# Performance work log

Hardware: AMD Instinct MI355X
Metric: run time of the kernel (lower is better)

## Reference

```python
import jax, jax.numpy as jnp
import numpy as np

EMB = 768
HEADS = 8
HEAD_DIM = EMB // HEADS
SCALE = HEAD_DIM ** -0.5


def setup_inputs() -> dict:
    key = jax.random.key(0)
    ks = jax.random.split(key, 9)
    s = 0.02
    return {
        "x": jax.random.normal(ks[0], (2, 4096, EMB), dtype=jnp.float32),
        "Wq": jax.random.normal(ks[1], (EMB, EMB), dtype=jnp.float32) * s,
        "bq": jax.random.normal(ks[2], (EMB,), dtype=jnp.float32) * s,
        "Wk": jax.random.normal(ks[3], (EMB, EMB), dtype=jnp.float32) * s,
        "bk": jax.random.normal(ks[4], (EMB,), dtype=jnp.float32) * s,
        "Wv": jax.random.normal(ks[5], (EMB, EMB), dtype=jnp.float32) * s,
        "bv": jax.random.normal(ks[6], (EMB,), dtype=jnp.float32) * s,
        "Wo": jax.random.normal(ks[7], (EMB, EMB), dtype=jnp.float32) * s,
        "bo": jax.random.normal(ks[8], (EMB,), dtype=jnp.float32) * s,
    }


def reference(x, Wq, bq, Wk, bk, Wv, bv, Wo, bo):
    b, n, _ = x.shape
    # torch Linear: y = x @ W.T + b
    def split_heads(y):  # [b, n, emb] -> [b, h, n, d]
        return y.reshape(b, n, HEADS, HEAD_DIM).transpose(0, 2, 1, 3)

    q = split_heads(x @ Wq.T + bq)
    k = split_heads(x @ Wk.T + bk)
    v = split_heads(x @ Wv.T + bv)
    # scores [b, h, q, k]; source applies scaling inside softmax input
    scores = jnp.einsum('bhqd,bhkd->bhqk', q, k) * SCALE
    weight = jax.nn.softmax(scores, axis=-1)
    out = jnp.einsum('bhqk,bhkd->bhqd', weight, v)
    out = out.transpose(0, 2, 1, 3).reshape(b, n, EMB)
    return out @ Wo.T + bo
```

## Files before the change

### kernel.cpp

```cpp
#include <hip/hip_runtime.h>


typedef __bf16 bf16;
typedef __attribute__((ext_vector_type(2))) float f32x2;
typedef __attribute__((ext_vector_type(4))) float f32x4;
typedef __attribute__((ext_vector_type(16))) float f32x16;
typedef __attribute__((ext_vector_type(8))) __bf16 bf16x8;
typedef __attribute__((ext_vector_type(4))) __bf16 bf16x4;
typedef __attribute__((ext_vector_type(4))) unsigned u32x4;

#define EMB 768
#define SEQ 4096
#define NB 2
#define NHEADS 8
#define HD 96
#define BHTOT (NB * NHEADS)
#define MTOT (NB * SEQ)
#define QSCALE 0.14724241052735512f

#define AS1 __attribute__((address_space(1)))
#define AS3 __attribute__((address_space(3)))

__global__ __launch_bounds__(256) void cast_f32_bf16(const float* __restrict__ in,
                                                     bf16* __restrict__ out) {
  const int i = (blockIdx.x * 256 + threadIdx.x) * 4;
  const f32x4 v = *reinterpret_cast<const f32x4*>(in + i);
  bf16x4 o;
  o[0] = (bf16)v[0]; o[1] = (bf16)v[1]; o[2] = (bf16)v[2]; o[3] = (bf16)v[3];
  *reinterpret_cast<bf16x4*>(out + i) = o;
}

__global__ __launch_bounds__(256) void cast_w4(const float* __restrict__ w0,
                                               const float* __restrict__ w1,
                                               const float* __restrict__ w2,
                                               const float* __restrict__ w3,
                                               bf16* __restrict__ o0,
                                               bf16* __restrict__ o1,
                                               bf16* __restrict__ o2,
                                               bf16* __restrict__ o3) {
  const float* w = (blockIdx.y == 0) ? w0 : (blockIdx.y == 1) ? w1 : (blockIdx.y == 2) ? w2 : w3;
  bf16* o = (blockIdx.y == 0) ? o0 : (blockIdx.y == 1) ? o1 : (blockIdx.y == 2) ? o2 : o3;
  const int i = (blockIdx.x * 256 + threadIdx.x) * 4;
  const f32x4 v = *reinterpret_cast<const f32x4*>(w + i);
  bf16x4 ob;
  ob[0] = (bf16)v[0]; ob[1] = (bf16)v[1]; ob[2] = (bf16)v[2]; ob[3] = (bf16)v[3];
  *reinterpret_cast<bf16x4*>(o + i) = ob;
}

template <int MODE>
__global__ __launch_bounds__(256) void gemm_bt(const bf16* __restrict__ A,
                                               const bf16* __restrict__ B,
                                               const float* __restrict__ b0,
                                               const float* __restrict__ b1,
                                               const float* __restrict__ b2,
                                               void* __restrict__ out,
                                               void* __restrict__ outK) {
  constexpr int K = EMB;
  __shared__ bf16 As[128 * 32];
  __shared__ bf16 Bs[128 * 32];
  const int tid = threadIdx.x;
  const int lane = tid & 63;
  const int wid = tid >> 6;
  const int wr = wid >> 1, wc = wid & 1;
  const int l15 = lane & 15, l4 = lane >> 4;
  const int rowBase = blockIdx.y * 128;
  const int colBase = blockIdx.x * 128;

  f32x4 acc[4][4] = {};

  for (int kt = 0; kt < K / 32; ++kt) {
    const int kb = kt * 32;
#pragma unroll
    for (int i = 0; i < 2; ++i) {
      const int c = (wid * 2 + i) * 64 + lane;
      const int row = c >> 2, cc = c & 3;
      const bf16* ga = A + (size_t)(rowBase + row) * K + kb + cc * 8;
      const bf16* gb = B + (size_t)(colBase + row) * K + kb + cc * 8;
      __builtin_amdgcn_global_load_lds(
          (const AS1 void*)ga,
          (AS3 void*)(As + (size_t)(wid * 2 + i) * 512), 16, 0, 0);
      __builtin_amdgcn_global_load_lds(
          (const AS1 void*)gb,
          (AS3 void*)(Bs + (size_t)(wid * 2 + i) * 512), 16, 0, 0);
    }
    __syncthreads();
    bf16x8 af[4], bfr[4];
#pragma unroll
    for (int t = 0; t < 4; ++t) {
      af[t]  = *reinterpret_cast<const bf16x8*>(As + (wr * 64 + t * 16 + l15) * 32 + l4 * 8);
      bfr[t] = *reinterpret_cast<const bf16x8*>(Bs + (wc * 64 + t * 16 + l15) * 32 + l4 * 8);
    }
#pragma unroll
    for (int mt = 0; mt < 4; ++mt)
#pragma unroll
      for (int nt = 0; nt < 4; ++nt)
        acc[mt][nt] = __builtin_amdgcn_mfma_f32_16x16x32_bf16(af[mt], bfr[nt], acc[mt][nt], 0, 0, 0);
    __syncthreads();
  }

#pragma unroll
  for (int mt = 0; mt < 4; ++mt) {
#pragma unroll
    for (int nt = 0; nt < 4; ++nt) {
      const int gn = colBase + wc * 64 + nt * 16 + l15;
      if (MODE == 0) {
        const int mm = gn / 768;
        const int g7 = gn - mm * 768;
        const int h = g7 / HD, d = g7 - h * HD;
        const float* bp = (mm == 0) ? b0 : (mm == 1) ? b1 : b2;
        const float bv = bp[g7];
        const float sc = (mm == 0) ? QSCALE : 1.f;
#pragma unroll
        for (int r = 0; r < 4; ++r) {
          const int gm = rowBase + wr * 64 + mt * 16 + l4 * 4 + r;
          const int b = gm >> 12, n = gm & (SEQ - 1);
          const float v = (acc[mt][nt][r] + bv) * sc;
          if (mm == 1) {
            ((bf16*)outK)[((size_t)(b * NHEADS + h) * SEQ + n) * 128 +
                          (((d >> 3) ^ (n & 7)) << 3) + (d & 7)] = (bf16)v;
          } else {
            bf16* dst = (bf16*)out + (mm == 2 ? (size_t)MTOT * EMB : 0);
            dst[((size_t)(b * NHEADS + h) * SEQ + n) * HD + d] = (bf16)v;
          }
        }
      } else {
        const float bv = b0[gn];
#pragma unroll
        for (int r = 0; r < 4; ++r) {
          const int gm = rowBase + wr * 64 + mt * 16 + l4 * 4 + r;
          ((float*)out)[(size_t)gm * EMB + gn] = acc[mt][nt][r] + bv;
        }
      }
    }
  }
}

__global__ __launch_bounds__(256) void transpose_v(const bf16* __restrict__ v,
                                                   bf16* __restrict__ vt) {
  __shared__ bf16 T[96][72];
  const int bh = blockIdx.y;
  const int n0 = blockIdx.x * 64;
  const int tid = threadIdx.x;
#pragma unroll
  for (int i = 0; i < 3; ++i) {
    const int c = i * 256 + tid;
    const int n = c / 12, cc = c % 12;
    const bf16x8 val = *reinterpret_cast<const bf16x8*>(
        v + ((size_t)bh * SEQ + n0 + n) * HD + cc * 8);
#pragma unroll
    for (int j = 0; j < 8; ++j) T[cc * 8 + j][n] = val[j];
  }
  __syncthreads();
#pragma unroll
  for (int i = 0; i < 3; ++i) {
    const int c = i * 256 + tid;
    const int d = c >> 3, nc = c & 7;
    const int s0i = (nc >> 1) * 16 + (nc & 1) * 4;
    const bf16x4 lo = *reinterpret_cast<const bf16x4*>(&T[d][s0i]);
    const bf16x4 hi = *reinterpret_cast<const bf16x4*>(&T[d][s0i + 8]);
    const bf16x8 val = __builtin_shufflevector(lo, hi, 0, 1, 2, 3, 4, 5, 6, 7);
    const int pc = nc ^ (d & 7);
    *reinterpret_cast<bf16x8*>(vt + ((size_t)bh * HD + d) * SEQ + n0 + pc * 8) = val;
  }
}

template <int SPLIT>
__global__ __launch_bounds__(256, 2) void attn_fwd(const bf16* __restrict__ q,
                                                   const bf16* __restrict__ ksw,
                                                   const bf16* __restrict__ vt,
                                                   void* __restrict__ outp,
                                                   float* __restrict__ lsum) {
  __shared__ bf16 Ks[2][64 * 128];
  __shared__ bf16 Vts[2][96 * 64];
  const int tid = threadIdx.x;
  const int lane = tid & 63;
  const int wid = tid >> 6;
  const int l31 = lane & 31, lhi = lane >> 5;
  const int lin = (blockIdx.z * gridDim.y + blockIdx.y) * gridDim.x + blockIdx.x;
  const int nblk = 256 * SPLIT;
  const int cpx = nblk >> 3;
  const int l2 = (lin & 7) * cpx + (lin >> 3);
  const int qblk = l2 & 15;
  const int z = (SPLIT == 2) ? ((l2 >> 4) & 1) : 0;
  const int bh = (SPLIT == 2) ? (l2 >> 5) : (l2 >> 4);
  const int q0 = qblk * 256 + wid * 64;
  constexpr int NT = SEQ / 64 / SPLIT;
  const int kv00 = z * NT * 64;
  const size_t headq = (size_t)bh * SEQ * HD;
  const bf16* kg = ksw + (size_t)bh * SEQ * 128;
  const bf16* vg = vt + (size_t)bh * (size_t)HD * SEQ;

  const bf16* kp = kg + (size_t)kv00 * 128 + (size_t)tid * 8;
  const bf16* vp = vg + (size_t)(tid >> 3) * SEQ + kv00 + (tid & 7) * 8;

  int krd[12], vrd[12];
#pragma unroll
  for (int kib = 0; kib < 2; ++kib)
#pragma unroll
    for (int dc = 0; dc < 6; ++dc) {
      const int row = kib * 32 + l31;
      krd[kib * 6 + dc] = (row * 128 + (((dc * 2 + lhi) ^ (l31 & 7)) * 8)) * 2;
    }
#pragma unroll
  for (int db = 0; db < 3; ++db)
#pragma unroll
    for (int kb = 0; kb < 4; ++kb) {
      const int row = db * 32 + l31;
      vrd[db * 4 + kb] = (row * 64 + (((kb * 2 + lhi) ^ (l31 & 7)) * 8)) * 2;
    }

  bf16x8 qf[2][6];
#pragma unroll
  for (int g = 0; g < 2; ++g)
#pragma unroll
    for (int dc = 0; dc < 6; ++dc)
      qf[g][dc] = *reinterpret_cast<const bf16x8*>(
          q + headq + (size_t)(q0 + g * 32 + l31) * HD + dc * 16 + lhi * 8);

  f32x16 oacc[2][3] = {};
  float lrun[2] = {0.f, 0.f};

#pragma unroll
  for (int i = 0; i < 4; ++i)
    __builtin_amdgcn_global_load_lds((const AS1 void*)(kp + i * 2048),
                                     (AS3 void*)(&Ks[0][i * 2048 + tid * 8]), 16, 0, 0);
#pragma unroll
  for (int i = 0; i < 3; ++i)
    __builtin_amdgcn_global_load_lds((const AS1 void*)(vp + (size_t)i * 32 * SEQ),
                                     (AS3 void*)(&Vts[0][i * 2048 + tid * 8]), 16, 0, 0);
  kp += 8192;
  vp += 64;
  __syncthreads();

  for (int kt = 0; kt < NT; ++kt) {
    const int cur = kt & 1;
    if (kt < NT - 1) {
#pragma unroll
      for (int i = 0; i < 4; ++i)
        __builtin_amdgcn_global_load_lds((const AS1 void*)(kp + i * 2048),
                                         (AS3 void*)(&Ks[cur ^ 1][i * 2048 + tid * 8]), 16, 0, 0);
#pragma unroll
      for (int i = 0; i < 3; ++i)
        __builtin_amdgcn_global_load_lds((const AS1 void*)(vp + (size_t)i * 32 * SEQ),
                                         (AS3 void*)(&Vts[cur ^ 1][i * 2048 + tid * 8]), 16, 0, 0);
      kp += 8192;
      vp += 64;
    }
    const char* ksb = (const char*)Ks[cur];
    const char* vsb = (const char*)Vts[cur];

    bf16x8 pf[2][4];
#pragma unroll
    for (int kib = 0; kib < 2; ++kib) {
      f32x16 s[2] = {};
      __builtin_amdgcn_s_setprio(1);
#pragma unroll
      for (int dc = 0; dc < 6; ++dc) {
        const bf16x8 kf = *reinterpret_cast<const bf16x8*>(ksb + krd[kib * 6 + dc]);
        s[0] = __builtin_amdgcn_mfma_f32_32x32x16_bf16(kf, qf[0][dc], s[0], 0, 0, 0);
        s[1] = __builtin_amdgcn_mfma_f32_32x32x16_bf16(kf, qf[1][dc], s[1], 0, 0, 0);
      }
      __builtin_amdgcn_s_setprio(0);
#pragma unroll
      for (int g = 0; g < 2; ++g) {
        float a0 = 0.f, a1 = 0.f, a2 = 0.f, a3 = 0.f;
#pragma unroll
        for (int i = 0; i < 4; ++i) {
          s[g][4 * i + 0] = __builtin_amdgcn_exp2f(s[g][4 * i + 0]); a0 += s[g][4 * i + 0];
          s[g][4 * i + 1] = __builtin_amdgcn_exp2f(s[g][4 * i + 1]); a1 += s[g][4 * i + 1];
          s[g][4 * i + 2] = __builtin_amdgcn_exp2f(s[g][4 * i + 2]); a2 += s[g][4 * i + 2];
          s[g][4 * i + 3] = __builtin_amdgcn_exp2f(s[g][4 * i + 3]); a3 += s[g][4 * i + 3];
        }
        lrun[g] += (a0 + a1) + (a2 + a3);
        unsigned c[8];
#pragma unroll
        for (int i = 0; i < 8; ++i)
          asm("v_cvt_pk_bf16_f32 %0, %1, %2"
              : "=v"(c[i]) : "v"(s[g][2 * i]), "v"(s[g][2 * i + 1]));
        const u32x4 wa = {c[0], c[1], c[2], c[3]};
        const u32x4 wb = {c[4], c[5], c[6], c[7]};
        pf[g][kib * 2 + 0] = __builtin_bit_cast(bf16x8, wa);
        pf[g][kib * 2 + 1] = __builtin_bit_cast(bf16x8, wb);
      }
    }

    __builtin_amdgcn_s_setprio(1);
#pragma unroll
    for (int kb = 0; kb < 4; ++kb) {
#pragma unroll
      for (int db = 0; db < 3; ++db) {
        const bf16x8 vf = *reinterpret_cast<const bf16x8*>(vsb + vrd[db * 4 + kb]);
        oacc[0][db] = __builtin_amdgcn_mfma_f32_32x32x16_bf16(vf, pf[0][kb], oacc[0][db], 0, 0, 0);
        oacc[1][db] = __builtin_amdgcn_mfma_f32_32x32x16_bf16(vf, pf[1][kb], oacc[1][db], 0, 0, 0);
      }
    }
    __builtin_amdgcn_s_setprio(0);

    __syncthreads();
  }

  const int b = bh >> 3, h = bh & 7;
#pragma unroll
  for (int g = 0; g < 2; ++g) {
    float lr = lrun[g];
    lr += __shfl_xor(lr, 32, 64);
    const int n = q0 + g * 32 + l31;
    if (SPLIT == 2) {
      float* po = (float*)outp + (size_t)z * ((size_t)BHTOT * SEQ * HD) +
                  ((size_t)bh * SEQ + n) * HD;
#pragma unroll
      for (int db = 0; db < 3; ++db)
#pragma unroll
        for (int i = 0; i < 8; ++i) {
          const int r = 2 * i;
          const int d = db * 32 + (r & 3) + 8 * (r >> 2) + 4 * lhi;
          f32x2 w = {oacc[g][db][r], oacc[g][db][r + 1]};
          *reinterpret_cast<f32x2*>(po + d) = w;
        }
      if (lhi == 0) lsum[(size_t)z * BHTOT * SEQ + (size_t)bh * SEQ + n] = lr;
    } else {
      const float inv = 1.f / lr;
      bf16* obase = (bf16*)outp + (size_t)(b * SEQ + n) * EMB + h * HD;
#pragma unroll
      for (int db = 0; db < 3; ++db)
#pragma unroll
        for (int i = 0; i < 8; ++i) {
          const int r = 2 * i;
          const int d = db * 32 + (r & 3) + 8 * (r >> 2) + 4 * lhi;
          unsigned w;
          const float v0 = oacc[g][db][r] * inv, v1 = oacc[g][db][r + 1] * inv;
          asm("v_cvt_pk_bf16_f32 %0, %1, %2" : "=v"(w) : "v"(v0), "v"(v1));
          *reinterpret_cast<unsigned*>(obase + d) = w;
        }
    }
  }
}

__global__ __launch_bounds__(256) void merge_o(const float* __restrict__ p,
                                               const float* __restrict__ ls,
                                               bf16* __restrict__ ao) {
  const int idx = blockIdx.x * 256 + threadIdx.x;
  const size_t PS = (size_t)BHTOT * SEQ * HD;
  const f32x4 a = *reinterpret_cast<const f32x4*>(p + (size_t)idx * 4);
  const f32x4 b2 = *reinterpret_cast<const f32x4*>(p + PS + (size_t)idx * 4);
  const int rest = idx / 24;
  const int d4 = idx - rest * 24;
  const float inv = 1.f / (ls[rest] + ls[BHTOT * SEQ + rest]);
  const int bh = rest >> 12, n = rest & (SEQ - 1);
  const int b = bh >> 3, h = bh & 7;
  bf16x4 o4;
#pragma unroll
  for (int j = 0; j < 4; ++j) o4[j] = (bf16)((a[j] + b2[j]) * inv);
  *reinterpret_cast<bf16x4*>(ao + (size_t)(b * SEQ + n) * EMB + h * HD + d4 * 4) = o4;
}

extern "C" void kernel_launch(void* const* d_in, const int* in_sizes, int n_in,
                              void* d_out, int out_size, void* d_ws, size_t ws_size,
                              hipStream_t stream) {
  const float* x  = (const float*)d_in[0];
  const float* Wq = (const float*)d_in[1];
  const float* bq = (const float*)d_in[2];
  const float* Wk = (const float*)d_in[3];
  const float* bk = (const float*)d_in[4];
  const float* Wv = (const float*)d_in[5];
  const float* bv = (const float*)d_in[6];
  const float* Wo = (const float*)d_in[7];
  const float* bo = (const float*)d_in[8];

  const size_t XN = (size_t)MTOT * EMB;
  const size_t WN = (size_t)EMB * EMB;
  const size_t KSWN = (size_t)BHTOT * SEQ * 128;

  bf16* p = (bf16*)d_ws;
  bf16* xbf  = p; p += XN;
  bf16* wqb  = p; p += WN;
  bf16* wkb  = p; p += WN;
  bf16* wvb  = p; p += WN;
  bf16* wob  = p; p += WN;
  bf16* qb   = p; p += XN;
  bf16* vb   = p; p += XN;
  bf16* kbsw = p; p += KSWN;
  bf16* vtb  = p; p += XN;
  bf16* ao   = p; p += XN;
  const size_t base_bytes = (size_t)((char*)p - (char*)d_ws);
  float* part = (float*)p;
  float* lsum = part + 2 * ((size_t)BHTOT * SEQ * HD);
  const size_t need2 = base_bytes + (2 * (size_t)BHTOT * SEQ * HD) * 4 +
                       (2 * (size_t)BHTOT * SEQ) * 4;
  const bool split2 = (ws_size >= need2);

  cast_f32_bf16<<<XN / 1024, 256, 0, stream>>>(x, xbf);
  cast_w4<<<dim3(WN / 1024, 4), 256, 0, stream>>>(Wq, Wk, Wv, Wo, wqb, wkb, wvb, wob);

  gemm_bt<0><<<dim3(3 * EMB / 128, MTOT / 128), 256, 0, stream>>>(
      xbf, wqb, bq, bk, bv, qb, kbsw);

  transpose_v<<<dim3(SEQ / 64, BHTOT), 256, 0, stream>>>(vb, vtb);

  if (split2) {
    attn_fwd<2><<<dim3(16, 16, 2), 256, 0, stream>>>(qb, kbsw, vtb, part, lsum);
    merge_o<<<(BHTOT * SEQ * HD / 4) / 256, 256, 0, stream>>>(part, lsum, ao);
  } else {
    attn_fwd<1><<<dim3(16, 16, 1), 256, 0, stream>>>(qb, kbsw, vtb, ao, nullptr);
  }

  gemm_bt<1><<<dim3(EMB / 128, MTOT / 128), 256, 0, stream>>>(
      ao, wob, bo, nullptr, nullptr, d_out, nullptr);
}
```

Baseline: 211.0 us.

## Halve attention KV tile to 32 and add 4-way KV split

Shrinks each attention iteration's K/V tile from 64 to 32 keys, with a matching V-transpose swizzle and LDS read offsets. This halves LDS use and registers per block. Adds a SPLIT=4 path, used when workspace allows, that splits the KV sequence across four blocks per query tile, and generalizes merge_o to sum four partials. The aim is more parallelism and occupancy, at the cost of twice as many barriers per key, more partial-output traffic and a heavier merge.

```diff
diff --git a/kernel.cpp b/kernel.cpp
--- a/kernel.cpp
+++ b/kernel.cpp
@@ -159,7 +159,7 @@
     const bf16x4 lo = *reinterpret_cast<const bf16x4*>(&T[d][s0i]);
     const bf16x4 hi = *reinterpret_cast<const bf16x4*>(&T[d][s0i + 8]);
     const bf16x8 val = __builtin_shufflevector(lo, hi, 0, 1, 2, 3, 4, 5, 6, 7);
-    const int pc = nc ^ (d & 7);
+    const int pc = (nc & 4) | ((nc & 3) ^ (d & 3));
     *reinterpret_cast<bf16x8*>(vt + ((size_t)bh * HD + d) * SEQ + n0 + pc * 8) = val;
   }
 }
@@ -170,43 +170,39 @@
                                                    const bf16* __restrict__ vt,
                                                    void* __restrict__ outp,
                                                    float* __restrict__ lsum) {
-  __shared__ bf16 Ks[2][64 * 128];
-  __shared__ bf16 Vts[2][96 * 64];
+  __shared__ bf16 Ks[2][32 * 128];
+  __shared__ bf16 Vts[2][96 * 32];
   const int tid = threadIdx.x;
   const int lane = tid & 63;
   const int wid = tid >> 6;
   const int l31 = lane & 31, lhi = lane >> 5;
   const int lin = (blockIdx.z * gridDim.y + blockIdx.y) * gridDim.x + blockIdx.x;
-  const int nblk = 256 * SPLIT;
-  const int cpx = nblk >> 3;
-  const int l2 = (lin & 7) * cpx + (lin >> 3);
+  constexpr int NBLK = 256 * SPLIT;
+  constexpr int CPX = NBLK >> 3;
+  const int l2 = (lin & 7) * CPX + (lin >> 3);
   const int qblk = l2 & 15;
-  const int z = (SPLIT == 2) ? ((l2 >> 4) & 1) : 0;
-  const int bh = (SPLIT == 2) ? (l2 >> 5) : (l2 >> 4);
+  const int z = (SPLIT == 4) ? ((l2 >> 4) & 3) : (SPLIT == 2) ? ((l2 >> 4) & 1) : 0;
+  const int bh = (SPLIT == 4) ? (l2 >> 6) : (SPLIT == 2) ? (l2 >> 5) : (l2 >> 4);
   const int q0 = qblk * 256 + wid * 64;
-  constexpr int NT = SEQ / 64 / SPLIT;
-  const int kv00 = z * NT * 64;
+  constexpr int NT = SEQ / 32 / SPLIT;
+  const int kv00 = z * NT * 32;
   const size_t headq = (size_t)bh * SEQ * HD;
   const bf16* kg = ksw + (size_t)bh * SEQ * 128;
   const bf16* vg = vt + (size_t)bh * (size_t)HD * SEQ;
 
   const bf16* kp = kg + (size_t)kv00 * 128 + (size_t)tid * 8;
-  const bf16* vp = vg + (size_t)(tid >> 3) * SEQ + kv00 + (tid & 7) * 8;
-
-  int krd[12], vrd[12];
-#pragma unroll
-  for (int kib = 0; kib < 2; ++kib)
-#pragma unroll
-    for (int dc = 0; dc < 6; ++dc) {
-      const int row = kib * 32 + l31;
-      krd[kib * 6 + dc] = (row * 128 + (((dc * 2 + lhi) ^ (l31 & 7)) * 8)) * 2;
-    }
+  const bf16* vp = vg + (size_t)(tid >> 2) * SEQ + kv00 + (tid & 3) * 8;
+
+  int krd[6], vrd[6];
+#pragma unroll
+  for (int dc = 0; dc < 6; ++dc)
+    krd[dc] = (l31 * 128 + (((dc * 2 + lhi) ^ (l31 & 7)) * 8)) * 2;
 #pragma unroll
   for (int db = 0; db < 3; ++db)
 #pragma unroll
-    for (int kb = 0; kb < 4; ++kb) {
+    for (int kb = 0; kb < 2; ++kb) {
       const int row = db * 32 + l31;
-      vrd[db * 4 + kb] = (row * 64 + (((kb * 2 + lhi) ^ (l31 & 7)) * 8)) * 2;
+      vrd[db * 2 + kb] = (row * 32 + (((kb * 2 + lhi) ^ (l31 & 3)) * 8)) * 2;
     }
 
   bf16x8 qf[2][6];
@@ -221,75 +217,75 @@
   float lrun[2] = {0.f, 0.f};
 
 #pragma unroll
-  for (int i = 0; i < 4; ++i)
+  for (int i = 0; i < 2; ++i)
     __builtin_amdgcn_global_load_lds((const AS1 void*)(kp + i * 2048),
                                      (AS3 void*)(&Ks[0][i * 2048 + tid * 8]), 16, 0, 0);
-#pragma unroll
-  for (int i = 0; i < 3; ++i)
-    __builtin_amdgcn_global_load_lds((const AS1 void*)(vp + (size_t)i * 32 * SEQ),
-                                     (AS3 void*)(&Vts[0][i * 2048 + tid * 8]), 16, 0, 0);
-  kp += 8192;
-  vp += 64;
+  __builtin_amdgcn_global_load_lds((const AS1 void*)(vp),
+                                   (AS3 void*)(&Vts[0][tid * 8]), 16, 0, 0);
+  if (tid < 128)
+    __builtin_amdgcn_global_load_lds((const AS1 void*)(vp + (size_t)64 * SEQ),
+                                     (AS3 void*)(&Vts[0][2048 + tid * 8]), 16, 0, 0);
+  kp += 4096;
+  vp += 32;
   __syncthreads();
 
   for (int kt = 0; kt < NT; ++kt) {
     const int cur = kt & 1;
     if (kt < NT - 1) {
 #pragma unroll
-      for (int i = 0; i < 4; ++i)
+      for (int i = 0; i < 2; ++i)
         __builtin_amdgcn_global_load_lds((const AS1 void*)(kp + i * 2048),
                                          (AS3 void*)(&Ks[cur ^ 1][i * 2048 + tid * 8]), 16, 0, 0);
-#pragma unroll
-      for (int i = 0; i < 3; ++i)
-        __builtin_amdgcn_global_load_lds((const AS1 void*)(vp + (size_t)i * 32 * SEQ),
-                                         (AS3 void*)(&Vts[cur ^ 1][i * 2048 + tid * 8]), 16, 0, 0);
-      kp += 8192;
-      vp += 64;
+      __builtin_amdgcn_global_load_lds((const AS1 void*)(vp),
+                                       (AS3 void*)(&Vts[cur ^ 1][tid * 8]), 16, 0, 0);
+      if (tid < 128)
+        __builtin_amdgcn_global_load_lds((const AS1 void*)(vp + (size_t)64 * SEQ),
+                                         (AS3 void*)(&Vts[cur ^ 1][2048 + tid * 8]), 16, 0, 0);
+      kp += 4096;
+      vp += 32;
     }
     const char* ksb = (const char*)Ks[cur];
     const char* vsb = (const char*)Vts[cur];
 
-    bf16x8 pf[2][4];
-#pragma unroll
-    for (int kib = 0; kib < 2; ++kib) {
-      f32x16 s[2] = {};
-      __builtin_amdgcn_s_setprio(1);
-#pragma unroll
-      for (int dc = 0; dc < 6; ++dc) {
-        const bf16x8 kf = *reinterpret_cast<const bf16x8*>(ksb + krd[kib * 6 + dc]);
-        s[0] = __builtin_amdgcn_mfma_f32_32x32x16_bf16(kf, qf[0][dc], s[0], 0, 0, 0);
-        s[1] = __builtin_amdgcn_mfma_f32_32x32x16_bf16(kf, qf[1][dc], s[1], 0, 0, 0);
+    f32x16 s[2] = {};
+    __builtin_amdgcn_s_setprio(1);
+#pragma unroll
+    for (int dc = 0; dc < 6; ++dc) {
+      const bf16x8 kf = *reinterpret_cast<const bf16x8*>(ksb + krd[dc]);
+      s[0] = __builtin_amdgcn_mfma_f32_32x32x16_bf16(kf, qf[0][dc], s[0], 0, 0, 0);
+      s[1] = __builtin_amdgcn_mfma_f32_32x32x16_bf16(kf, qf[1][dc], s[1], 0, 0, 0);
+    }
+    __builtin_amdgcn_s_setprio(0);
+
+    bf16x8 pf[2][2];
+#pragma unroll
+    for (int g = 0; g < 2; ++g) {
+      float a0 = 0.f, a1 = 0.f, a2 = 0.f, a3 = 0.f;
+#pragma unroll
+      for (int i = 0; i < 4; ++i) {
+        s[g][4 * i + 0] = __builtin_amdgcn_exp2f(s[g][4 * i + 0]); a0 += s[g][4 * i + 0];
+        s[g][4 * i + 1] = __builtin_amdgcn_exp2f(s[g][4 * i + 1]); a1 += s[g][4 * i + 1];
+        s[g][4 * i + 2] = __builtin_amdgcn_exp2f(s[g][4 * i + 2]); a2 += s[g][4 * i + 2];
+        s[g][4 * i + 3] = __builtin_amdgcn_exp2f(s[g][4 * i + 3]); a3 += s[g][4 * i + 3];
       }
-      __builtin_amdgcn_s_setprio(0);
-#pragma unroll
-      for (int g = 0; g < 2; ++g) {
-        float a0 = 0.f, a1 = 0.f, a2 = 0.f, a3 = 0.f;
-#pragma unroll
-        for (int i = 0; i < 4; ++i) {
-          s[g][4 * i + 0] = __builtin_amdgcn_exp2f(s[g][4 * i + 0]); a0 += s[g][4 * i + 0];
-          s[g][4 * i + 1] = __builtin_amdgcn_exp2f(s[g][4 * i + 1]); a1 += s[g][4 * i + 1];
-          s[g][4 * i + 2] = __builtin_amdgcn_exp2f(s[g][4 * i + 2]); a2 += s[g][4 * i + 2];
-          s[g][4 * i + 3] = __builtin_amdgcn_exp2f(s[g][4 * i + 3]); a3 += s[g][4 * i + 3];
-        }
-        lrun[g] += (a0 + a1) + (a2 + a3);
-        unsigned c[8];
-#pragma unroll
-        for (int i = 0; i < 8; ++i)
-          asm("v_cvt_pk_bf16_f32 %0, %1, %2"
-              : "=v"(c[i]) : "v"(s[g][2 * i]), "v"(s[g][2 * i + 1]));
-        const u32x4 wa = {c[0], c[1], c[2], c[3]};
-        const u32x4 wb = {c[4], c[5], c[6], c[7]};
-        pf[g][kib * 2 + 0] = __builtin_bit_cast(bf16x8, wa);
-        pf[g][kib * 2 + 1] = __builtin_bit_cast(bf16x8, wb);
-      }
+      lrun[g] += (a0 + a1) + (a2 + a3);
+      unsigned c[8];
+#pragma unroll
+      for (int i = 0; i < 8; ++i)
+        asm("v_cvt_pk_bf16_f32 %0, %1, %2"
+            : "=v"(c[i]) : "v"(s[g][2 * i]), "v"(s[g][2 * i + 1]));
+      const u32x4 wa = {c[0], c[1], c[2], c[3]};
+      const u32x4 wb = {c[4], c[5], c[6], c[7]};
+      pf[g][0] = __builtin_bit_cast(bf16x8, wa);
+      pf[g][1] = __builtin_bit_cast(bf16x8, wb);
     }
 
     __builtin_amdgcn_s_setprio(1);
 #pragma unroll
-    for (int kb = 0; kb < 4; ++kb) {
+    for (int kb = 0; kb < 2; ++kb) {
 #pragma unroll
       for (int db = 0; db < 3; ++db) {
-        const bf16x8 vf = *reinterpret_cast<const bf16x8*>(vsb + vrd[db * 4 + kb]);
+        const bf16x8 vf = *reinterpret_cast<const bf16x8*>(vsb + vrd[db * 2 + kb]);
         oacc[0][db] = __builtin_amdgcn_mfma_f32_32x32x16_bf16(vf, pf[0][kb], oacc[0][db], 0, 0, 0);
         oacc[1][db] = __builtin_amdgcn_mfma_f32_32x32x16_bf16(vf, pf[1][kb], oacc[1][db], 0, 0, 0);
       }
@@ -305,7 +301,7 @@
     float lr = lrun[g];
     lr += __shfl_xor(lr, 32, 64);
     const int n = q0 + g * 32 + l31;
-    if (SPLIT == 2) {
+    if (SPLIT > 1) {
       float* po = (float*)outp + (size_t)z * ((size_t)BHTOT * SEQ * HD) +
                   ((size_t)bh * SEQ + n) * HD;
 #pragma unroll
@@ -336,21 +332,29 @@
   }
 }
 
+template <int SPLIT>
 __global__ __launch_bounds__(256) void merge_o(const float* __restrict__ p,
                                                const float* __restrict__ ls,
                                                bf16* __restrict__ ao) {
   const int idx = blockIdx.x * 256 + threadIdx.x;
   const size_t PS = (size_t)BHTOT * SEQ * HD;
-  const f32x4 a = *reinterpret_cast<const f32x4*>(p + (size_t)idx * 4);
-  const f32x4 b2 = *reinterpret_cast<const f32x4*>(p + PS + (size_t)idx * 4);
   const int rest = idx / 24;
   const int d4 = idx - rest * 24;
-  const float inv = 1.f / (ls[rest] + ls[BHTOT * SEQ + rest]);
+  f32x4 a = *reinterpret_cast<const f32x4*>(p + (size_t)idx * 4);
+  float l = ls[rest];
+#pragma unroll
+  for (int zz = 1; zz < SPLIT; ++zz) {
+    const f32x4 b2 = *reinterpret_cast<const f32x4*>(p + zz * PS + (size_t)idx * 4);
+#pragma unroll
+    for (int j = 0; j < 4; ++j) a[j] += b2[j];
+    l += ls[(size_t)zz * BHTOT * SEQ + rest];
+  }
+  const float inv = 1.f / l;
   const int bh = rest >> 12, n = rest & (SEQ - 1);
   const int b = bh >> 3, h = bh & 7;
   bf16x4 o4;
 #pragma unroll
-  for (int j = 0; j < 4; ++j) o4[j] = (bf16)((a[j] + b2[j]) * inv);
+  for (int j = 0; j < 4; ++j) o4[j] = (bf16)(a[j] * inv);
   *reinterpret_cast<bf16x4*>(ao + (size_t)(b * SEQ + n) * EMB + h * HD + d4 * 4) = o4;
 }
 
@@ -384,10 +388,11 @@
   bf16* ao   = p; p += XN;
   const size_t base_bytes = (size_t)((char*)p - (char*)d_ws);
   float* part = (float*)p;
-  float* lsum = part + 2 * ((size_t)BHTOT * SEQ * HD);
-  const size_t need2 = base_bytes + (2 * (size_t)BHTOT * SEQ * HD) * 4 +
-                       (2 * (size_t)BHTOT * SEQ) * 4;
-  const bool split2 = (ws_size >= need2);
+  const size_t PS = (size_t)BHTOT * SEQ * HD;
+  float* lsum4 = part + 4 * PS;
+  float* lsum2 = part + 2 * PS;
+  const size_t need4 = base_bytes + 4 * PS * 4 + 4 * (size_t)BHTOT * SEQ * 4;
+  const size_t need2 = base_bytes + 2 * PS * 4 + 2 * (size_t)BHTOT * SEQ * 4;
 
   cast_f32_bf16<<<XN / 1024, 256, 0, stream>>>(x, xbf);
   cast_w4<<<dim3(WN / 1024, 4), 256, 0, stream>>>(Wq, Wk, Wv, Wo, wqb, wkb, wvb, wob);
@@ -397,9 +402,12 @@
 
   transpose_v<<<dim3(SEQ / 64, BHTOT), 256, 0, stream>>>(vb, vtb);
 
-  if (split2) {
-    attn_fwd<2><<<dim3(16, 16, 2), 256, 0, stream>>>(qb, kbsw, vtb, part, lsum);
-    merge_o<<<(BHTOT * SEQ * HD / 4) / 256, 256, 0, stream>>>(part, lsum, ao);
+  if (ws_size >= need4) {
+    attn_fwd<4><<<dim3(16, 16, 4), 256, 0, stream>>>(qb, kbsw, vtb, part, lsum4);
+    merge_o<4><<<(BHTOT * SEQ * HD / 4) / 256, 256, 0, stream>>>(part, lsum4, ao);
+  } else if (ws_size >= need2) {
+    attn_fwd<2><<<dim3(16, 16, 2), 256, 0, stream>>>(qb, kbsw, vtb, part, lsum2);
+    merge_o<2><<<(BHTOT * SEQ * HD / 4) / 256, 256, 0, stream>>>(part, lsum2, ao);
   } else {
     attn_fwd<1><<<dim3(16, 16, 1), 256, 0, stream>>>(qb, kbsw, vtb, ao, nullptr);
   }
```

Result: slower. 233.8 us (+10.8%).

## Software-pipeline QK and PV across KV tiles, triple-buffer V, store bf16 partials

Applied to the files above, without the earlier changes.

Restructures the attention inner loop so each half-tile's QK^T MFMAs are interleaved with the softmax and PV of the previous half-tile, with V moved to a triple buffer so its loads can be issued two tiles ahead. Precomputed LDS offset arrays are dropped and offsets are computed inline. Split-KV partial outputs are now stored as bf16 instead of fp32, halving partial-write and merge traffic, and the merge kernel is vectorised to 8 elements per thread. This costs extra LDS and register pressure and reduces partial-sum precision.

```diff
diff --git a/kernel.cpp b/kernel.cpp
--- a/kernel.cpp
+++ b/kernel.cpp
@@ -2,7 +2,6 @@
 
 
 typedef __bf16 bf16;
-typedef __attribute__((ext_vector_type(2))) float f32x2;
 typedef __attribute__((ext_vector_type(4))) float f32x4;
 typedef __attribute__((ext_vector_type(16))) float f32x16;
 typedef __attribute__((ext_vector_type(8))) __bf16 bf16x8;
@@ -171,15 +170,15 @@
                                                    void* __restrict__ outp,
                                                    float* __restrict__ lsum) {
   __shared__ bf16 Ks[2][64 * 128];
-  __shared__ bf16 Vts[2][96 * 64];
+  __shared__ bf16 Vts[3][96 * 64];
   const int tid = threadIdx.x;
   const int lane = tid & 63;
   const int wid = tid >> 6;
   const int l31 = lane & 31, lhi = lane >> 5;
   const int lin = (blockIdx.z * gridDim.y + blockIdx.y) * gridDim.x + blockIdx.x;
-  const int nblk = 256 * SPLIT;
-  const int cpx = nblk >> 3;
-  const int l2 = (lin & 7) * cpx + (lin >> 3);
+  constexpr int NBLK = 256 * SPLIT;
+  constexpr int CPX = NBLK >> 3;
+  const int l2 = (lin & 7) * CPX + (lin >> 3);
   const int qblk = l2 & 15;
   const int z = (SPLIT == 2) ? ((l2 >> 4) & 1) : 0;
   const int bh = (SPLIT == 2) ? (l2 >> 5) : (l2 >> 4);
@@ -193,22 +192,6 @@
   const bf16* kp = kg + (size_t)kv00 * 128 + (size_t)tid * 8;
   const bf16* vp = vg + (size_t)(tid >> 3) * SEQ + kv00 + (tid & 7) * 8;
 
-  int krd[12], vrd[12];
-#pragma unroll
-  for (int kib = 0; kib < 2; ++kib)
-#pragma unroll
-    for (int dc = 0; dc < 6; ++dc) {
-      const int row = kib * 32 + l31;
-      krd[kib * 6 + dc] = (row * 128 + (((dc * 2 + lhi) ^ (l31 & 7)) * 8)) * 2;
-    }
-#pragma unroll
-  for (int db = 0; db < 3; ++db)
-#pragma unroll
-    for (int kb = 0; kb < 4; ++kb) {
-      const int row = db * 32 + l31;
-      vrd[db * 4 + kb] = (row * 64 + (((kb * 2 + lhi) ^ (l31 & 7)) * 8)) * 2;
-    }
-
   bf16x8 qf[2][6];
 #pragma unroll
   for (int g = 0; g < 2; ++g)
@@ -220,83 +203,109 @@
   f32x16 oacc[2][3] = {};
   float lrun[2] = {0.f, 0.f};
 
-#pragma unroll
-  for (int i = 0; i < 4; ++i)
-    __builtin_amdgcn_global_load_lds((const AS1 void*)(kp + i * 2048),
-                                     (AS3 void*)(&Ks[0][i * 2048 + tid * 8]), 16, 0, 0);
-#pragma unroll
-  for (int i = 0; i < 3; ++i)
-    __builtin_amdgcn_global_load_lds((const AS1 void*)(vp + (size_t)i * 32 * SEQ),
-                                     (AS3 void*)(&Vts[0][i * 2048 + tid * 8]), 16, 0, 0);
-  kp += 8192;
-  vp += 64;
+  auto STAGE_K = [&](int buf) {
+#pragma unroll
+    for (int i = 0; i < 4; ++i)
+      __builtin_amdgcn_global_load_lds((const AS1 void*)(kp + i * 2048),
+                                       (AS3 void*)(&Ks[buf][i * 2048 + tid * 8]), 16, 0, 0);
+    kp += 8192;
+  };
+  auto STAGE_V = [&](int buf) {
+#pragma unroll
+    for (int i = 0; i < 3; ++i)
+      __builtin_amdgcn_global_load_lds((const AS1 void*)(vp + (size_t)i * 32 * SEQ),
+                                       (AS3 void*)(&Vts[buf][i * 2048 + tid * 8]), 16, 0, 0);
+    vp += 64;
+  };
+  auto QKSTEP = [&](const bf16* ksb_, int kib, f32x16& s0, f32x16& s1) {
+    const char* ksb = (const char*)ksb_;
+    __builtin_amdgcn_s_setprio(1);
+#pragma unroll
+    for (int dc = 0; dc < 6; ++dc) {
+      const int off = ((kib * 32 + l31) * 128 + (((dc * 2 + lhi) ^ (l31 & 7)) * 8)) * 2;
+      const bf16x8 kf = *reinterpret_cast<const bf16x8*>(ksb + off);
+      s0 = __builtin_amdgcn_mfma_f32_32x32x16_bf16(kf, qf[0][dc], s0, 0, 0, 0);
+      s1 = __builtin_amdgcn_mfma_f32_32x32x16_bf16(kf, qf[1][dc], s1, 0, 0, 0);
+    }
+    __builtin_amdgcn_s_setprio(0);
+  };
+  auto SMPV = [&](const bf16* vsb_, int kib, f32x16& c0, f32x16& c1) {
+    const char* vsb = (const char*)vsb_;
+    bf16x8 vf[2][3];
+#pragma unroll
+    for (int kb = 0; kb < 2; ++kb)
+#pragma unroll
+      for (int db = 0; db < 3; ++db) {
+        const int off = ((db * 32 + l31) * 64 +
+                         ((((kib * 2 + kb) * 2 + lhi) ^ (l31 & 7)) * 8)) * 2;
+        vf[kb][db] = *reinterpret_cast<const bf16x8*>(vsb + off);
+      }
+    bf16x8 pf0[2], pf1[2];
+    {
+      float a0 = 0.f, a1 = 0.f, a2 = 0.f, a3 = 0.f;
+#pragma unroll
+      for (int i = 0; i < 4; ++i) {
+        c0[4 * i + 0] = __builtin_amdgcn_exp2f(c0[4 * i + 0]); a0 += c0[4 * i + 0];
+        c0[4 * i + 1] = __builtin_amdgcn_exp2f(c0[4 * i + 1]); a1 += c0[4 * i + 1];
+        c0[4 * i + 2] = __builtin_amdgcn_exp2f(c0[4 * i + 2]); a2 += c0[4 * i + 2];
+        c0[4 * i + 3] = __builtin_amdgcn_exp2f(c0[4 * i + 3]); a3 += c0[4 * i + 3];
+      }
+      lrun[0] += (a0 + a1) + (a2 + a3);
+      unsigned c[8];
+#pragma unroll
+      for (int i = 0; i < 8; ++i)
+        asm("v_cvt_pk_bf16_f32 %0, %1, %2" : "=v"(c[i]) : "v"(c0[2 * i]), "v"(c0[2 * i + 1]));
+      const u32x4 wa = {c[0], c[1], c[2], c[3]};
+      const u32x4 wb = {c[4], c[5], c[6], c[7]};
+      pf0[0] = __builtin_bit_cast(bf16x8, wa);
+      pf0[1] = __builtin_bit_cast(bf16x8, wb);
+    }
+    {
+      float a0 = 0.f, a1 = 0.f, a2 = 0.f, a3 = 0.f;
+#pragma unroll
+      for (int i = 0; i < 4; ++i) {
+        c1[4 * i + 0] = __builtin_amdgcn_exp2f(c1[4 * i + 0]); a0 += c1[4 * i + 0];
+        c1[4 * i + 1] = __builtin_amdgcn_exp2f(c1[4 * i + 1]); a1 += c1[4 * i + 1];
+        c1[4 * i + 2] = __builtin_amdgcn_exp2f(c1[4 * i + 2]); a2 += c1[4 * i + 2];
+        c1[4 * i + 3] = __builtin_amdgcn_exp2f(c1[4 * i + 3]); a3 += c1[4 * i + 3];
+      }
+      lrun[1] += (a0 + a1) + (a2 + a3);
+      unsigned c[8];
+#pragma unroll
+      for (int i = 0; i < 8; ++i)
+        asm("v_cvt_pk_bf16_f32 %0, %1, %2" : "=v"(c[i]) : "v"(c1[2 * i]), "v"(c1[2 * i + 1]));
+      const u32x4 wa = {c[0], c[1], c[2], c[3]};
+      const u32x4 wb = {c[4], c[5], c[6], c[7]};
+      pf1[0] = __builtin_bit_cast(bf16x8, wa);
+      pf1[1] = __builtin_bit_cast(bf16x8, wb);
+    }
+    __builtin_amdgcn_s_setprio(1);
+#pragma unroll
+    for (int kb = 0; kb < 2; ++kb)
+#pragma unroll
+      for (int db = 0; db < 3; ++db) {
+        oacc[0][db] = __builtin_amdgcn_mfma_f32_32x32x16_bf16(vf[kb][db], pf0[kb], oacc[0][db], 0, 0, 0);
+        oacc[1][db] = __builtin_amdgcn_mfma_f32_32x32x16_bf16(vf[kb][db], pf1[kb], oacc[1][db], 0, 0, 0);
+      }
+    __builtin_amdgcn_s_setprio(0);
+  };
+
+  STAGE_K(0); STAGE_V(0);
   __syncthreads();
-
-  for (int kt = 0; kt < NT; ++kt) {
-    const int cur = kt & 1;
-    if (kt < NT - 1) {
-#pragma unroll
-      for (int i = 0; i < 4; ++i)
-        __builtin_amdgcn_global_load_lds((const AS1 void*)(kp + i * 2048),
-                                         (AS3 void*)(&Ks[cur ^ 1][i * 2048 + tid * 8]), 16, 0, 0);
-#pragma unroll
-      for (int i = 0; i < 3; ++i)
-        __builtin_amdgcn_global_load_lds((const AS1 void*)(vp + (size_t)i * 32 * SEQ),
-                                         (AS3 void*)(&Vts[cur ^ 1][i * 2048 + tid * 8]), 16, 0, 0);
-      kp += 8192;
-      vp += 64;
-    }
-    const char* ksb = (const char*)Ks[cur];
-    const char* vsb = (const char*)Vts[cur];
-
-    bf16x8 pf[2][4];
-#pragma unroll
-    for (int kib = 0; kib < 2; ++kib) {
-      f32x16 s[2] = {};
-      __builtin_amdgcn_s_setprio(1);
-#pragma unroll
-      for (int dc = 0; dc < 6; ++dc) {
-        const bf16x8 kf = *reinterpret_cast<const bf16x8*>(ksb + krd[kib * 6 + dc]);
-        s[0] = __builtin_amdgcn_mfma_f32_32x32x16_bf16(kf, qf[0][dc], s[0], 0, 0, 0);
-        s[1] = __builtin_amdgcn_mfma_f32_32x32x16_bf16(kf, qf[1][dc], s[1], 0, 0, 0);
-      }
-      __builtin_amdgcn_s_setprio(0);
-#pragma unroll
-      for (int g = 0; g < 2; ++g) {
-        float a0 = 0.f, a1 = 0.f, a2 = 0.f, a3 = 0.f;
-#pragma unroll
-        for (int i = 0; i < 4; ++i) {
-          s[g][4 * i + 0] = __builtin_amdgcn_exp2f(s[g][4 * i + 0]); a0 += s[g][4 * i + 0];
-          s[g][4 * i + 1] = __builtin_amdgcn_exp2f(s[g][4 * i + 1]); a1 += s[g][4 * i + 1];
-          s[g][4 * i + 2] = __builtin_amdgcn_exp2f(s[g][4 * i + 2]); a2 += s[g][4 * i + 2];
-          s[g][4 * i + 3] = __builtin_amdgcn_exp2f(s[g][4 * i + 3]); a3 += s[g][4 * i + 3];
-        }
-        lrun[g] += (a0 + a1) + (a2 + a3);
-        unsigned c[8];
-#pragma unroll
-        for (int i = 0; i < 8; ++i)
-          asm("v_cvt_pk_bf16_f32 %0, %1, %2"
-              : "=v"(c[i]) : "v"(s[g][2 * i]), "v"(s[g][2 * i + 1]));
-        const u32x4 wa = {c[0], c[1], c[2], c[3]};
-        const u32x4 wb = {c[4], c[5], c[6], c[7]};
-        pf[g][kib * 2 + 0] = __builtin_bit_cast(bf16x8, wa);
-        pf[g][kib * 2 + 1] = __builtin_bit_cast(bf16x8, wb);
-      }
-    }
-
-    __builtin_amdgcn_s_setprio(1);
-#pragma unroll
-    for (int kb = 0; kb < 4; ++kb) {
-#pragma unroll
-      for (int db = 0; db < 3; ++db) {
-        const bf16x8 vf = *reinterpret_cast<const bf16x8*>(vsb + vrd[db * 4 + kb]);
-        oacc[0][db] = __builtin_amdgcn_mfma_f32_32x32x16_bf16(vf, pf[0][kb], oacc[0][db], 0, 0, 0);
-        oacc[1][db] = __builtin_amdgcn_mfma_f32_32x32x16_bf16(vf, pf[1][kb], oacc[1][db], 0, 0, 0);
-      }
-    }
-    __builtin_amdgcn_s_setprio(0);
-
+  f32x16 sA0 = {}, sA1 = {}, sB0 = {}, sB1 = {};
+  QKSTEP(Ks[0], 0, sA0, sA1);
+  STAGE_K(1); STAGE_V(1);
+
+  for (int t = 0; t < NT; ++t) {
+    const int vb = t % 3;
+    sB0 = (f32x16){}; sB1 = (f32x16){};
+    QKSTEP(Ks[t & 1], 1, sB0, sB1);
+    SMPV(Vts[vb], 0, sA0, sA1);
     __syncthreads();
+    if (t + 2 < NT) { STAGE_K(t & 1); STAGE_V((t + 2) % 3); }
+    sA0 = (f32x16){}; sA1 = (f32x16){};
+    if (t + 1 < NT) QKSTEP(Ks[(t + 1) & 1], 0, sA0, sA1);
+    SMPV(Vts[vb], 1, sB0, sB1);
   }
 
   const int b = bh >> 3, h = bh & 7;
@@ -306,16 +315,18 @@
     lr += __shfl_xor(lr, 32, 64);
     const int n = q0 + g * 32 + l31;
     if (SPLIT == 2) {
-      float* po = (float*)outp + (size_t)z * ((size_t)BHTOT * SEQ * HD) +
-                  ((size_t)bh * SEQ + n) * HD;
+      bf16* po = (bf16*)outp + (size_t)z * ((size_t)BHTOT * SEQ * HD) +
+                 ((size_t)bh * SEQ + n) * HD;
 #pragma unroll
       for (int db = 0; db < 3; ++db)
 #pragma unroll
         for (int i = 0; i < 8; ++i) {
           const int r = 2 * i;
           const int d = db * 32 + (r & 3) + 8 * (r >> 2) + 4 * lhi;
-          f32x2 w = {oacc[g][db][r], oacc[g][db][r + 1]};
-          *reinterpret_cast<f32x2*>(po + d) = w;
+          unsigned w;
+          asm("v_cvt_pk_bf16_f32 %0, %1, %2"
+              : "=v"(w) : "v"(oacc[g][db][r]), "v"(oacc[g][db][r + 1]));
+          *reinterpret_cast<unsigned*>(po + d) = w;
         }
       if (lhi == 0) lsum[(size_t)z * BHTOT * SEQ + (size_t)bh * SEQ + n] = lr;
     } else {
@@ -336,22 +347,22 @@
   }
 }
 
-__global__ __launch_bounds__(256) void merge_o(const float* __restrict__ p,
+__global__ __launch_bounds__(256) void merge_o(const bf16* __restrict__ p,
                                                const float* __restrict__ ls,
                                                bf16* __restrict__ ao) {
   const int idx = blockIdx.x * 256 + threadIdx.x;
   const size_t PS = (size_t)BHTOT * SEQ * HD;
-  const f32x4 a = *reinterpret_cast<const f32x4*>(p + (size_t)idx * 4);
-  const f32x4 b2 = *reinterpret_cast<const f32x4*>(p + PS + (size_t)idx * 4);
-  const int rest = idx / 24;
-  const int d4 = idx - rest * 24;
+  const int rest = idx / 12;
+  const int d8 = idx - rest * 12;
+  const bf16x8 a = *reinterpret_cast<const bf16x8*>(p + (size_t)idx * 8);
+  const bf16x8 b2 = *reinterpret_cast<const bf16x8*>(p + PS + (size_t)idx * 8);
   const float inv = 1.f / (ls[rest] + ls[BHTOT * SEQ + rest]);
   const int bh = rest >> 12, n = rest & (SEQ - 1);
   const int b = bh >> 3, h = bh & 7;
-  bf16x4 o4;
-#pragma unroll
-  for (int j = 0; j < 4; ++j) o4[j] = (bf16)((a[j] + b2[j]) * inv);
-  *reinterpret_cast<bf16x4*>(ao + (size_t)(b * SEQ + n) * EMB + h * HD + d4 * 4) = o4;
+  bf16x8 o8;
+#pragma unroll
+  for (int j = 0; j < 8; ++j) o8[j] = (bf16)(((float)a[j] + (float)b2[j]) * inv);
+  *reinterpret_cast<bf16x8*>(ao + (size_t)(b * SEQ + n) * EMB + h * HD + d8 * 8) = o8;
 }
 
 extern "C" void kernel_launch(void* const* d_in, const int* in_sizes, int n_in,
@@ -383,10 +394,10 @@
   bf16* vtb  = p; p += XN;
   bf16* ao   = p; p += XN;
   const size_t base_bytes = (size_t)((char*)p - (char*)d_ws);
-  float* part = (float*)p;
-  float* lsum = part + 2 * ((size_t)BHTOT * SEQ * HD);
-  const size_t need2 = base_bytes + (2 * (size_t)BHTOT * SEQ * HD) * 4 +
-                       (2 * (size_t)BHTOT * SEQ) * 4;
+  const size_t PS = (size_t)BHTOT * SEQ * HD;
+  bf16* part = p;
+  float* lsum = (float*)(p + 2 * PS);
+  const size_t need2 = base_bytes + 2 * PS * 2 + 2 * (size_t)BHTOT * SEQ * 4;
   const bool split2 = (ws_size >= need2);
 
   cast_f32_bf16<<<XN / 1024, 256, 0, stream>>>(x, xbf);
@@ -399,7 +410,7 @@
 
   if (split2) {
     attn_fwd<2><<<dim3(16, 16, 2), 256, 0, stream>>>(qb, kbsw, vtb, part, lsum);
-    merge_o<<<(BHTOT * SEQ * HD / 4) / 256, 256, 0, stream>>>(part, lsum, ao);
+    merge_o<<<(int)(PS / 8 / 256), 256, 0, stream>>>(part, lsum, ao);
   } else {
     attn_fwd<1><<<dim3(16, 16, 1), 256, 0, stream>>>(qb, kbsw, vtb, ao, nullptr);
   }
```

New measurement: 239.3 us (median of 3 runs). +13.4%, slower.
